# Performance work log

Measured on AMD Instinct MI355X. Metric: run time of the kernel, lower is better.

## Reference

```python
import jax, jax.numpy as jnp
import numpy as np

ENC_DIM = 128
DEC_DIM = 128
NUM_HEADS = 4
HEAD_DIM = DEC_DIM // NUM_HEADS


def _layernorm(x, g, b, eps=1e-5):
    mu = jnp.mean(x, axis=-1, keepdims=True)
    var = jnp.mean((x - mu) ** 2, axis=-1, keepdims=True)
    return (x - mu) * jax.lax.rsqrt(var + eps) * g + b


def setup_inputs() -> dict:
    key = jax.random.key(0)
    ks = jax.random.split(key, 12)
    B, H, W, D = 2, 16, 16, 16
    s = 0.02
    return {
        "encoder_feat": jax.random.normal(ks[0], (B, ENC_DIM, H, W, D), jnp.float32),
        "decoder_feat": jax.random.normal(ks[1], (B, DEC_DIM, H, W, D), jnp.float32),
        # torch Linear weights stored as [out, in]
        "Wq": jax.random.normal(ks[2], (DEC_DIM, DEC_DIM), jnp.float32) * s,
        "bq": jnp.zeros((DEC_DIM,), jnp.float32),
        "Wk": jax.random.normal(ks[3], (DEC_DIM, ENC_DIM), jnp.float32) * s,
        "bk": jnp.zeros((DEC_DIM,), jnp.float32),
        "Wv": jax.random.normal(ks[4], (DEC_DIM, ENC_DIM), jnp.float32) * s,
        "bv": jnp.zeros((DEC_DIM,), jnp.float32),
        "Wo": jax.random.normal(ks[5], (DEC_DIM, DEC_DIM), jnp.float32) * s,
        "bo": jnp.zeros((DEC_DIM,), jnp.float32),
        "g_enc": jnp.ones((ENC_DIM,), jnp.float32),
        "b_enc": jnp.zeros((ENC_DIM,), jnp.float32),
        "g_dec": jnp.ones((DEC_DIM,), jnp.float32),
        "b_dec": jnp.zeros((DEC_DIM,), jnp.float32),
        "g_out": jnp.ones((DEC_DIM,), jnp.float32),
        "b_out": jnp.zeros((DEC_DIM,), jnp.float32),
        "W1": jax.random.normal(ks[6], (DEC_DIM * 4, DEC_DIM), jnp.float32) * s,
        "b1": jnp.zeros((DEC_DIM * 4,), jnp.float32),
        "W2": jax.random.normal(ks[7], (DEC_DIM, DEC_DIM * 4), jnp.float32) * s,
        "b2": jnp.zeros((DEC_DIM,), jnp.float32),
    }


def reference(encoder_feat, decoder_feat, Wq, bq, Wk, bk, Wv, bv, Wo, bo,
              g_enc, b_enc, g_dec, b_dec, g_out, b_out, W1, b1, W2, b2):
    B, C_dec, H, W_, D = decoder_feat.shape
    N = H * W_ * D
    scale = HEAD_DIM ** -0.5
    # [B, C, H, W, D] -> [B, N, C]
    enc_seq = encoder_feat.reshape(B, -1, N).transpose(0, 2, 1)
    dec_seq = decoder_feat.reshape(B, C_dec, N).transpose(0, 2, 1)
    enc_seq = _layernorm(enc_seq, g_enc, b_enc)
    dec_seq = _layernorm(dec_seq, g_dec, b_dec)
    # projections (torch Linear: x @ W.T + b), split heads -> [B, h, N, d]
    Q = (dec_seq @ Wq.T + bq).reshape(B, N, NUM_HEADS, HEAD_DIM).transpose(0, 2, 1, 3)
    K = (enc_seq @ Wk.T + bk).reshape(B, N, NUM_HEADS, HEAD_DIM).transpose(0, 2, 1, 3)
    V = (enc_seq @ Wv.T + bv).reshape(B, N, NUM_HEADS, HEAD_DIM).transpose(0, 2, 1, 3)
    attn = jnp.einsum('bhqd,bhkd->bhqk', Q, K) * scale  # [B, h, N, N]
    attn = jax.nn.softmax(attn, axis=-1)
    out = jnp.einsum('bhqk,bhkd->bhqd', attn, V)
    out = out.transpose(0, 2, 1, 3).reshape(B, N, C_dec)
    out = out @ Wo.T + bo
    out = dec_seq + out
    h = _layernorm(out, g_out, b_out)
    ffn = jax.nn.gelu(h @ W1.T + b1, approximate=False) @ W2.T + b2
    out = out + ffn
    return out.transpose(0, 2, 1).reshape(B, C_dec, H, W_, D)
```

## Files before the change

kernel.cpp:

```cpp
#include <hip/hip_runtime.h>
#include <hip/hip_bf16.h>
#include <math.h>

#define B_ 2
#define N_ 4096
#define BN_ 8192
#define NH_ 4
#define SPLIT_ 8

using bf16x8   = __attribute__((ext_vector_type(8))) __bf16;
using f32x4    = __attribute__((ext_vector_type(4))) float;
using ushortx8 = __attribute__((ext_vector_type(8))) unsigned short;

#if __has_builtin(__builtin_amdgcn_exp2f)
#define FAST_EXP2(x) __builtin_amdgcn_exp2f(x)
#else
#define FAST_EXP2(x) __expf((x) * 0.6931471805599453f)
#endif

static __device__ __forceinline__ unsigned short f2bf(float f) {
    union { __hip_bfloat16 h; unsigned short u; } c;
    c.h = __float2bfloat16(f);
    return c.u;
}
static __device__ __forceinline__ float bf2f(unsigned short u) {
    union { __hip_bfloat16 h; unsigned short u; } c;
    c.u = u;
    return __bfloat162float(c.h);
}
static __device__ __forceinline__ unsigned int pk2bf(float lo, float hi) {
    return __builtin_amdgcn_perm(__float_as_uint(hi) + 0x8000u,
                                 __float_as_uint(lo) + 0x8000u, 0x07060302u);
}

__global__ __launch_bounds__(256)
void qkv4_kernel(const float* __restrict__ enc, const float* __restrict__ dec,
                 const float* __restrict__ g_enc, const float* __restrict__ b_enc,
                 const float* __restrict__ g_dec, const float* __restrict__ b_dec,
                 const float* __restrict__ Wq, const float* __restrict__ Wk,
                 const float* __restrict__ Wv,
                 const float* __restrict__ bq, const float* __restrict__ bk,
                 const float* __restrict__ bv,
                 const float* __restrict__ Wo, const float* __restrict__ W1,
                 const float* __restrict__ W2,
                 unsigned short* __restrict__ wo, unsigned short* __restrict__ w1,
                 unsigned short* __restrict__ w2,
                 unsigned short* __restrict__ Qh, unsigned short* __restrict__ Kh,
                 unsigned short* __restrict__ Vt,
                 unsigned short* __restrict__ dec_lnb) {
    const int t = threadIdx.x;
    if (blockIdx.x >= 768) {
        const int e = ((int)blockIdx.x - 768) * 2048 + t * 8;
        const float* src; unsigned short* dst; int off;
        if (e < 16384)       { src = Wo; dst = wo; off = e; }
        else if (e < 81920)  { src = W1; dst = w1; off = e - 16384; }
        else                 { src = W2; dst = w2; off = e - 81920; }
        const float4 a = *(const float4*)(src + off);
        const float4 b = *(const float4*)(src + off + 4);
        uint4 p;
        p.x = pk2bf(a.x, a.y); p.y = pk2bf(a.z, a.w);
        p.z = pk2bf(b.x, b.y); p.w = pk2bf(b.z, b.w);
        *(uint4*)(dst + off) = p;
        return;
    }
    __shared__ float tile[128][33];
    __shared__ float mu_s[32], inv_s[32];
    __shared__ alignas(16) unsigned short Wlds[128][136];
    const int z  = blockIdx.x >> 8;
    const int m0 = (blockIdx.x & 255) * 32;
    const int b  = m0 >> 12, n0 = m0 & 4095;
    const float* inb   = ((z == 0) ? dec : enc) + (size_t)b * 128 * N_;
    const float* gamma = (z == 0) ? g_dec : g_enc;
    const float* beta  = (z == 0) ? b_dec : b_enc;
    const float* Wb    = (z == 0) ? Wq : ((z == 1) ? Wk : Wv);

    {
        const int col = t & 31;
        const int r0  = t >> 5;
        #pragma unroll
        for (int j = 0; j < 16; ++j) {
            const int r = r0 + 8 * j;
            tile[r][col] = inb[(size_t)r * N_ + n0 + col];
        }
    }
    {
        #pragma unroll
        for (int i = 0; i < 8; ++i) {
            const int e   = (i * 256 + t) * 8;
            const int col = e >> 7, k = e & 127;
            const float4 wa = *(const float4*)(Wb + e);
            const float4 wb = *(const float4*)(Wb + e + 4);
            uint4 p;
            p.x = pk2bf(wa.x, wa.y); p.y = pk2bf(wa.z, wa.w);
            p.z = pk2bf(wb.x, wb.y); p.w = pk2bf(wb.z, wb.w);
            *(uint4*)&Wlds[col][k] = p;
        }
    }
    __syncthreads();
    {
        const int tok = t >> 3;
        const int ln  = t & 7;
        float s = 0.f, ss = 0.f;
        for (int c = ln; c < 128; c += 8) {
            const float x = tile[c][tok];
            s += x; ss += x * x;
        }
        for (int m = 1; m < 8; m <<= 1) {
            s  += __shfl_xor(s, m);
            ss += __shfl_xor(ss, m);
        }
        if (ln == 0) {
            const float mu  = s * (1.f / 128.f);
            mu_s[tok]  = mu;
            inv_s[tok] = rsqrtf(ss * (1.f / 128.f) - mu * mu + 1e-5f);
        }
    }
    __syncthreads();

    const int wvx = t >> 6, lane = t & 63;
    const int l15 = lane & 15, quad = lane >> 4;
    const int tokgrp  = (wvx & 1) * 16;
    const int colbase = (wvx >> 1) * 64;
    const bool wrLN   = (z == 0) && ((wvx >> 1) == 0);
    const int tok = tokgrp + l15;
    const float mu  = mu_s[tok];
    const float inv = inv_s[tok];

    bf16x8 af[4];
    #pragma unroll
    for (int kk = 0; kk < 4; ++kk) {
        float y[8];
        #pragma unroll
        for (int j = 0; j < 8; ++j) {
            const int c = kk * 32 + quad * 8 + j;
            y[j] = (tile[c][tok] - mu) * inv * gamma[c] + beta[c];
        }
        union { uint4 u; bf16x8 v8; ushortx8 us; } cvt;
        cvt.u.x = pk2bf(y[0], y[1]); cvt.u.y = pk2bf(y[2], y[3]);
        cvt.u.z = pk2bf(y[4], y[5]); cvt.u.w = pk2bf(y[6], y[7]);
        af[kk] = cvt.v8;
        if (wrLN)
            *(ushortx8*)(dec_lnb + (size_t)(m0 + tok) * 128 + kk * 32 + quad * 8) = cvt.us;
    }

    const float* bias = (z == 0) ? bq : ((z == 1) ? bk : bv);
    const float sc = (z == 0) ? (0.17677669529663687f * 1.4426950408889634f) : 1.f;
    const int nbase = n0 + tokgrp + quad * 4;

    #pragma unroll
    for (int nb = 0; nb < 4; ++nb) {
        const int col = colbase + nb * 16 + l15;
        f32x4 a = {0.f, 0.f, 0.f, 0.f};
        #pragma unroll
        for (int kk = 0; kk < 4; ++kk) {
            const bf16x8 wf = *(const bf16x8*)&Wlds[col][kk * 32 + quad * 8];
            a = __builtin_amdgcn_mfma_f32_16x16x32_bf16(af[kk], wf, a, 0, 0, 0);
        }
        const int h = col >> 5, d = col & 31;
        const float bz = bias[col];
        if (z == 2) {
            ushort4 pk;
            pk.x = f2bf(a[0] + bz);
            pk.y = f2bf(a[1] + bz);
            pk.z = f2bf(a[2] + bz);
            pk.w = f2bf(a[3] + bz);
            *(ushort4*)(Vt + ((size_t)(b * NH_ + h) * 32 + d) * N_ + nbase) = pk;
        } else {
            unsigned short* dst = (z == 0) ? Qh : Kh;
            #pragma unroll
            for (int r = 0; r < 4; ++r)
                dst[((size_t)(b * NH_ + h) * N_ + nbase + r) * 32 + d] = f2bf((a[r] + bz) * sc);
        }
    }
}

__global__ __launch_bounds__(512)
void attn_kernel7(const unsigned short* __restrict__ Qh,
                  const unsigned short* __restrict__ Kh,
                  const unsigned short* __restrict__ Vt,
                  unsigned short* __restrict__ ctx) {
    __shared__ alignas(16) unsigned short sP[8][64][72];
    __shared__ float ldsL[8][64];

    const int gid  = blockIdx.x;
    const int bh   = gid & 7;
    const int qblk = gid >> 3;
    const int t  = threadIdx.x;
    const int wvx = t >> 6, lane = t & 63;
    const int l15 = lane & 15, quad = lane >> 4;
    const int s = wvx;
    const int qw = qblk * 64;
    const size_t hbse = (size_t)bh * N_ * 32;

    bf16x8 qf[4];
    #pragma unroll
    for (int f = 0; f < 4; ++f)
        qf[f] = *(const bf16x8*)(Qh + hbse + (size_t)(qw + f * 16 + l15) * 32 + quad * 8);

    const unsigned short* Kp = Kh + hbse;
    const unsigned short* Vp = Vt + (size_t)bh * 32 * N_;

    f32x4 o0[4], o1[4];
    float l[4];
    #pragma unroll
    for (int f = 0; f < 4; ++f) {
        o0[f] = f32x4{0.f, 0.f, 0.f, 0.f};
        o1[f] = f32x4{0.f, 0.f, 0.f, 0.f};
        l[f] = 0.f;
    }
    const f32x4 zero = {0.f, 0.f, 0.f, 0.f};

    const int kbeg = s * (N_ / SPLIT_);
    const int kend = kbeg + (N_ / SPLIT_);

    bf16x8 kf[4];
    #pragma unroll
    for (int c = 0; c < 4; ++c)
        kf[c] = *(const bf16x8*)(Kp + (size_t)(kbeg + c * 16 + l15) * 32 + quad * 8);

    for (int k0 = kbeg; k0 < kend; k0 += 64) {
        bf16x8 va[2], vb[2];
        #pragma unroll
        for (int s2 = 0; s2 < 2; ++s2) {
            va[s2] = *(const bf16x8*)(Vp + (size_t)l15 * N_        + k0 + s2 * 32 + quad * 8);
            vb[s2] = *(const bf16x8*)(Vp + (size_t)(16 + l15) * N_ + k0 + s2 * 32 + quad * 8);
        }
        const int kn = (k0 + 64 < kend) ? (k0 + 64) : kbeg;
        bf16x8 kfn[4];
        #pragma unroll
        for (int c = 0; c < 4; ++c)
            kfn[c] = *(const bf16x8*)(Kp + (size_t)(kn + c * 16 + l15) * 32 + quad * 8);

        __builtin_amdgcn_s_setprio(1);
        #pragma unroll
        for (int f = 0; f < 4; ++f) {
            #pragma unroll
            for (int c = 0; c < 4; ++c) {
                const f32x4 sv = __builtin_amdgcn_mfma_f32_16x16x32_bf16(kf[c], qf[f], zero, 0, 0, 0);
                const float p0 = FAST_EXP2(sv[0]);
                const float p1 = FAST_EXP2(sv[1]);
                const float p2 = FAST_EXP2(sv[2]);
                const float p3 = FAST_EXP2(sv[3]);
                l[f] += (p0 + p1) + (p2 + p3);
                uint2 pk;
                pk.x = pk2bf(p0, p1);
                pk.y = pk2bf(p2, p3);
                *(uint2*)&sP[wvx][f * 16 + l15][c * 16 + quad * 4] = pk;
            }
        }
        __builtin_amdgcn_s_setprio(0);
        __builtin_amdgcn_s_setprio(1);
        #pragma unroll
        for (int f = 0; f < 4; ++f) {
            #pragma unroll
            for (int s2 = 0; s2 < 2; ++s2) {
                const bf16x8 pf = *(const bf16x8*)&sP[wvx][f * 16 + l15][s2 * 32 + quad * 8];
                o0[f] = __builtin_amdgcn_mfma_f32_16x16x32_bf16(va[s2], pf, o0[f], 0, 0, 0);
                o1[f] = __builtin_amdgcn_mfma_f32_16x16x32_bf16(vb[s2], pf, o1[f], 0, 0, 0);
            }
        }
        __builtin_amdgcn_s_setprio(0);
        #pragma unroll
        for (int c = 0; c < 4; ++c) kf[c] = kfn[c];
    }

    float lf4[4];
    #pragma unroll
    for (int f = 0; f < 4; ++f) {
        float lf = l[f];
        lf += __shfl_xor(lf, 16);
        lf += __shfl_xor(lf, 32);
        lf4[f] = lf;
    }

    __syncthreads();
    float* ldsO = (float*)&sP[0][0][0];
    #pragma unroll
    for (int f = 0; f < 4; ++f) {
        const int q = f * 16 + l15;
        float* row = ldsO + ((size_t)s * 64 + q) * 36;
        *(f32x4*)(row + quad * 4)      = o0[f];
        *(f32x4*)(row + 16 + quad * 4) = o1[f];
        if (quad == 0) ldsL[s][q] = lf4[f];
    }
    __syncthreads();

    const int tok = t >> 3;
    const int d0  = (t & 7) * 4;
    f32x4 sum = {0.f, 0.f, 0.f, 0.f};
    float lsum = 0.f;
    #pragma unroll
    for (int w = 0; w < 8; ++w) {
        sum  += *(const f32x4*)(ldsO + ((size_t)w * 64 + tok) * 36 + d0);
        lsum += ldsL[w][tok];
    }
    const float inv = 1.f / lsum;
    uint2 pk;
    pk.x = pk2bf(sum[0] * inv, sum[1] * inv);
    pk.y = pk2bf(sum[2] * inv, sum[3] * inv);
    const int b = bh >> 2, h = bh & 3;
    *(uint2*)(ctx + ((size_t)(b * N_ + qw + tok)) * 128 + h * 32 + d0) = pk;
}

__global__ __launch_bounds__(256)
void fused_tail4_kernel(const unsigned short* __restrict__ ctx,
                        const unsigned short* __restrict__ wo,
                        const float* __restrict__ bo,
                        const unsigned short* __restrict__ decb,
                        const float* __restrict__ g, const float* __restrict__ be,
                        const unsigned short* __restrict__ w1,
                        const float* __restrict__ b1,
                        const unsigned short* __restrict__ w2,
                        const float* __restrict__ b2,
                        float* __restrict__ out) {
    __shared__ alignas(16) unsigned short sredb[4][64][36];
    __shared__ float sln[4][2][16];
    __shared__ alignas(16) unsigned short hb_lds[16][136];
    __shared__ alignas(16) unsigned short smid[16][536];
    const int t = threadIdx.x;
    const int wv = t >> 6, lane = t & 63;
    const int l15 = lane & 15, quad = lane >> 4;
    const int m0 = blockIdx.x * 16;

    const int tokA = m0 + l15;
    const bf16x8 af = *(const bf16x8*)(ctx + (size_t)tokA * 128 + wv * 32 + quad * 8);

    #pragma unroll
    for (int nb = 0; nb < 8; ++nb) {
        const bf16x8 wf = *(const bf16x8*)(wo + (size_t)(nb * 16 + l15) * 128
                                           + wv * 32 + quad * 8);
        const f32x4 a = __builtin_amdgcn_mfma_f32_16x16x32_bf16(
            af, wf, f32x4{0.f, 0.f, 0.f, 0.f}, 0, 0, 0);
        uint2 p;
        p.x = pk2bf(a[0], a[1]);
        p.y = pk2bf(a[2], a[3]);
        *(uint2*)&sredb[wv][lane][nb * 4] = p;
    }
    __syncthreads();

    float v[2][4];
    #pragma unroll
    for (int lnb = 0; lnb < 2; ++lnb) {
        const int nbg = 2 * wv + lnb;
        f32x4 p = {0.f, 0.f, 0.f, 0.f};
        #pragma unroll
        for (int w = 0; w < 4; ++w) {
            const ushort4 u = *(const ushort4*)&sredb[w][lane][nbg * 4];
            p[0] += bf2f(u.x); p[1] += bf2f(u.y);
            p[2] += bf2f(u.z); p[3] += bf2f(u.w);
        }
        const int col = nbg * 16 + l15;
        const float bz = bo[col];
        #pragma unroll
        for (int r = 0; r < 4; ++r) {
            const int tok = m0 + quad * 4 + r;
            v[lnb][r] = p[r] + bz + bf2f(decb[(size_t)tok * 128 + col]);
        }
    }

    {
        float s[4], ss[4];
        #pragma unroll
        for (int r = 0; r < 4; ++r) {
            float a = v[0][r] + v[1][r];
            float b = v[0][r] * v[0][r] + v[1][r] * v[1][r];
            for (int m = 1; m < 16; m <<= 1) {
                a += __shfl_xor(a, m);
                b += __shfl_xor(b, m);
            }
            s[r] = a; ss[r] = b;
        }
        if (l15 == 0) {
            #pragma unroll
            for (int r = 0; r < 4; ++r) {
                sln[wv][0][quad * 4 + r] = s[r];
                sln[wv][1][quad * 4 + r] = ss[r];
            }
        }
    }
    __syncthreads();

    {
        #pragma unroll
        for (int r = 0; r < 4; ++r) {
            const int tk = quad * 4 + r;
            const float stot  = sln[0][0][tk] + sln[1][0][tk] + sln[2][0][tk] + sln[3][0][tk];
            const float sstot = sln[0][1][tk] + sln[1][1][tk] + sln[2][1][tk] + sln[3][1][tk];
            const float mu  = stot * (1.f / 128.f);
            const float inv = rsqrtf(sstot * (1.f / 128.f) - mu * mu + 1e-5f);
            #pragma unroll
            for (int lnb = 0; lnb < 2; ++lnb) {
                const int col = (2 * wv + lnb) * 16 + l15;
                hb_lds[tk][col] = f2bf((v[lnb][r] - mu) * inv * g[col] + be[col]);
            }
        }
    }
    __syncthreads();

    bf16x8 hf[4];
    #pragma unroll
    for (int kk = 0; kk < 4; ++kk)
        hf[kk] = *(const bf16x8*)&hb_lds[l15][kk * 32 + quad * 8];
    #pragma unroll
    for (int nb = 0; nb < 8; ++nb) {
        const int col = wv * 128 + nb * 16 + l15;
        f32x4 a = {0.f, 0.f, 0.f, 0.f};
        #pragma unroll
        for (int kk = 0; kk < 4; ++kk) {
            const bf16x8 wf = *(const bf16x8*)(w1 + (size_t)col * 128 + kk * 32 + quad * 8);
            a = __builtin_amdgcn_mfma_f32_16x16x32_bf16(hf[kk], wf, a, 0, 0, 0);
        }
        const float bz = b1[col];
        #pragma unroll
        for (int r = 0; r < 4; ++r) {
            float x = a[r] + bz;
            x = 0.5f * x * (1.f + erff(x * 0.70710678118f));
            smid[quad * 4 + r][col] = f2bf(x);
        }
    }
    __syncthreads();

    f32x4 acc[8];
    #pragma unroll
    for (int nb = 0; nb < 8; ++nb) acc[nb] = f32x4{0.f, 0.f, 0.f, 0.f};
    #pragma unroll
    for (int kk = 0; kk < 4; ++kk) {
        const bf16x8 af2 = *(const bf16x8*)&smid[l15][wv * 128 + kk * 32 + quad * 8];
        #pragma unroll
        for (int nb = 0; nb < 8; ++nb) {
            const bf16x8 wf = *(const bf16x8*)(w2 + (size_t)(nb * 16 + l15) * 512
                                               + wv * 128 + kk * 32 + quad * 8);
            acc[nb] = __builtin_amdgcn_mfma_f32_16x16x32_bf16(af2, wf, acc[nb], 0, 0, 0);
        }
    }
    __syncthreads();
    #pragma unroll
    for (int nb = 0; nb < 8; ++nb) {
        uint2 p;
        p.x = pk2bf(acc[nb][0], acc[nb][1]);
        p.y = pk2bf(acc[nb][2], acc[nb][3]);
        *(uint2*)&sredb[wv][lane][nb * 4] = p;
    }
    __syncthreads();

    {
        const int b = m0 >> 12;
        const int nb0 = (m0 & 4095) + quad * 4;
        #pragma unroll
        for (int lnb = 0; lnb < 2; ++lnb) {
            const int nbg = 2 * wv + lnb;
            f32x4 p = {0.f, 0.f, 0.f, 0.f};
            #pragma unroll
            for (int w = 0; w < 4; ++w) {
                const ushort4 u = *(const ushort4*)&sredb[w][lane][nbg * 4];
                p[0] += bf2f(u.x); p[1] += bf2f(u.y);
                p[2] += bf2f(u.z); p[3] += bf2f(u.w);
            }
            const int col = nbg * 16 + l15;
            const float bz = b2[col];
            f32x4 res;
            #pragma unroll
            for (int r = 0; r < 4; ++r)
                res[r] = p[r] + bz + v[lnb][r];
            *(f32x4*)&out[((size_t)(b * 128 + col)) * N_ + nb0] = res;
        }
    }
}

extern "C" void kernel_launch(void* const* d_in, const int* in_sizes, int n_in,
                              void* d_out, int out_size, void* d_ws, size_t ws_size,
                              hipStream_t stream) {
    const float* enc   = (const float*)d_in[0];
    const float* dec   = (const float*)d_in[1];
    const float* Wq    = (const float*)d_in[2];
    const float* bq    = (const float*)d_in[3];
    const float* Wk    = (const float*)d_in[4];
    const float* bk    = (const float*)d_in[5];
    const float* Wv    = (const float*)d_in[6];
    const float* bv    = (const float*)d_in[7];
    const float* Wo    = (const float*)d_in[8];
    const float* bo    = (const float*)d_in[9];
    const float* g_enc = (const float*)d_in[10];
    const float* b_enc = (const float*)d_in[11];
    const float* g_dec = (const float*)d_in[12];
    const float* b_dec = (const float*)d_in[13];
    const float* g_out = (const float*)d_in[14];
    const float* b_out = (const float*)d_in[15];
    const float* W1    = (const float*)d_in[16];
    const float* b1    = (const float*)d_in[17];
    const float* W2    = (const float*)d_in[18];
    const float* b2    = (const float*)d_in[19];
    float* out = (float*)d_out;
    char*  W   = (char*)d_ws;

    unsigned short* wob = (unsigned short*)(W);
    unsigned short* w1b = wob + 16384;
    unsigned short* w2b = w1b + 65536;
    unsigned short* dec_lnb = (unsigned short*)(W + (2560ull << 10));
    unsigned short* Qh      = (unsigned short*)(W + (4608ull << 10));
    unsigned short* Kh      = (unsigned short*)(W + (6656ull << 10));
    unsigned short* Vt      = (unsigned short*)(W + (8704ull << 10));
    unsigned short* ctx     = (unsigned short*)(W + (10752ull << 10));

    qkv4_kernel<<<768 + 72, 256, 0, stream>>>(
        enc, dec, g_enc, b_enc, g_dec, b_dec, Wq, Wk, Wv, bq, bk, bv,
        Wo, W1, W2, wob, w1b, w2b, Qh, Kh, Vt, dec_lnb);

    attn_kernel7<<<512, 512, 0, stream>>>(Qh, Kh, Vt, ctx);

    fused_tail4_kernel<<<512, 256, 0, stream>>>(ctx, wob, bo, dec_lnb,
                                                g_out, b_out, w1b, b1, w2b, b2, out);
}
```

Baseline: 157.1 us.

## Split tail GEMMs by output columns, fold weight conversion into QKV blocks

The tail kernel now has each wave own two output column blocks across the full K dimension for both the Wo and W2 GEMMs. This removes the split-K LDS reduction buffer, its bf16 round-trips and the extra barriers. The weight bf16 conversion is spread over the 768 QKV blocks, 24 threads each, instead of 72 extra blocks. The input tile load switches to float4 vector reads. In exchange, each wave now loads more weight data from global memory.

```diff
diff --git a/kernel.cpp b/kernel.cpp
--- a/kernel.cpp
+++ b/kernel.cpp
@@ -49,20 +49,6 @@
                  unsigned short* __restrict__ Vt,
                  unsigned short* __restrict__ dec_lnb) {
     const int t = threadIdx.x;
-    if (blockIdx.x >= 768) {
-        const int e = ((int)blockIdx.x - 768) * 2048 + t * 8;
-        const float* src; unsigned short* dst; int off;
-        if (e < 16384)       { src = Wo; dst = wo; off = e; }
-        else if (e < 81920)  { src = W1; dst = w1; off = e - 16384; }
-        else                 { src = W2; dst = w2; off = e - 81920; }
-        const float4 a = *(const float4*)(src + off);
-        const float4 b = *(const float4*)(src + off + 4);
-        uint4 p;
-        p.x = pk2bf(a.x, a.y); p.y = pk2bf(a.z, a.w);
-        p.z = pk2bf(b.x, b.y); p.w = pk2bf(b.z, b.w);
-        *(uint4*)(dst + off) = p;
-        return;
-    }
     __shared__ float tile[128][33];
     __shared__ float mu_s[32], inv_s[32];
     __shared__ alignas(16) unsigned short Wlds[128][136];
@@ -74,13 +60,29 @@
     const float* beta  = (z == 0) ? b_dec : b_enc;
     const float* Wb    = (z == 0) ? Wq : ((z == 1) ? Wk : Wv);
 
-    {
-        const int col = t & 31;
-        const int r0  = t >> 5;
-        #pragma unroll
-        for (int j = 0; j < 16; ++j) {
-            const int r = r0 + 8 * j;
-            tile[r][col] = inb[(size_t)r * N_ + n0 + col];
+    if (t < 24) {
+        const int e = (int)blockIdx.x * 192 + t * 8;
+        const float* src; unsigned short* dst; int off;
+        if (e < 16384)       { src = Wo; dst = wo; off = e; }
+        else if (e < 81920)  { src = W1; dst = w1; off = e - 16384; }
+        else                 { src = W2; dst = w2; off = e - 81920; }
+        const float4 a = *(const float4*)(src + off);
+        const float4 bq4 = *(const float4*)(src + off + 4);
+        uint4 p;
+        p.x = pk2bf(a.x, a.y); p.y = pk2bf(a.z, a.w);
+        p.z = pk2bf(bq4.x, bq4.y); p.w = pk2bf(bq4.z, bq4.w);
+        *(uint4*)(dst + off) = p;
+    }
+
+    {
+        const int r0 = t >> 3;
+        const int cf = (t & 7) * 4;
+        #pragma unroll
+        for (int j = 0; j < 4; ++j) {
+            const int r = r0 + 32 * j;
+            const float4 x = *(const float4*)(inb + (size_t)r * N_ + n0 + cf);
+            tile[r][cf]     = x.x; tile[r][cf + 1] = x.y;
+            tile[r][cf + 2] = x.z; tile[r][cf + 3] = x.w;
         }
     }
     {
@@ -303,7 +305,7 @@
 }
 
 __global__ __launch_bounds__(256)
-void fused_tail4_kernel(const unsigned short* __restrict__ ctx,
+void fused_tail5_kernel(const unsigned short* __restrict__ ctx,
                         const unsigned short* __restrict__ wo,
                         const float* __restrict__ bo,
                         const unsigned short* __restrict__ decb,
@@ -313,7 +315,6 @@
                         const unsigned short* __restrict__ w2,
                         const float* __restrict__ b2,
                         float* __restrict__ out) {
-    __shared__ alignas(16) unsigned short sredb[4][64][36];
     __shared__ float sln[4][2][16];
     __shared__ alignas(16) unsigned short hb_lds[16][136];
     __shared__ alignas(16) unsigned short smid[16][536];
@@ -322,39 +323,26 @@
     const int l15 = lane & 15, quad = lane >> 4;
     const int m0 = blockIdx.x * 16;
 
-    const int tokA = m0 + l15;
-    const bf16x8 af = *(const bf16x8*)(ctx + (size_t)tokA * 128 + wv * 32 + quad * 8);
-
-    #pragma unroll
-    for (int nb = 0; nb < 8; ++nb) {
-        const bf16x8 wf = *(const bf16x8*)(wo + (size_t)(nb * 16 + l15) * 128
-                                           + wv * 32 + quad * 8);
-        const f32x4 a = __builtin_amdgcn_mfma_f32_16x16x32_bf16(
-            af, wf, f32x4{0.f, 0.f, 0.f, 0.f}, 0, 0, 0);
-        uint2 p;
-        p.x = pk2bf(a[0], a[1]);
-        p.y = pk2bf(a[2], a[3]);
-        *(uint2*)&sredb[wv][lane][nb * 4] = p;
-    }
-    __syncthreads();
+    bf16x8 af[4];
+    #pragma unroll
+    for (int kk = 0; kk < 4; ++kk)
+        af[kk] = *(const bf16x8*)(ctx + (size_t)(m0 + l15) * 128 + kk * 32 + quad * 8);
 
     float v[2][4];
     #pragma unroll
     for (int lnb = 0; lnb < 2; ++lnb) {
-        const int nbg = 2 * wv + lnb;
-        f32x4 p = {0.f, 0.f, 0.f, 0.f};
-        #pragma unroll
-        for (int w = 0; w < 4; ++w) {
-            const ushort4 u = *(const ushort4*)&sredb[w][lane][nbg * 4];
-            p[0] += bf2f(u.x); p[1] += bf2f(u.y);
-            p[2] += bf2f(u.z); p[3] += bf2f(u.w);
-        }
-        const int col = nbg * 16 + l15;
+        const int col = (2 * wv + lnb) * 16 + l15;
+        f32x4 a = {0.f, 0.f, 0.f, 0.f};
+        #pragma unroll
+        for (int kk = 0; kk < 4; ++kk) {
+            const bf16x8 wf = *(const bf16x8*)(wo + (size_t)col * 128 + kk * 32 + quad * 8);
+            a = __builtin_amdgcn_mfma_f32_16x16x32_bf16(af[kk], wf, a, 0, 0, 0);
+        }
         const float bz = bo[col];
         #pragma unroll
         for (int r = 0; r < 4; ++r) {
             const int tok = m0 + quad * 4 + r;
-            v[lnb][r] = p[r] + bz + bf2f(decb[(size_t)tok * 128 + col]);
+            v[lnb][r] = a[r] + bz + bf2f(decb[(size_t)tok * 128 + col]);
         }
     }
 
@@ -420,48 +408,31 @@
     }
     __syncthreads();
 
-    f32x4 acc[8];
-    #pragma unroll
-    for (int nb = 0; nb < 8; ++nb) acc[nb] = f32x4{0.f, 0.f, 0.f, 0.f};
-    #pragma unroll
-    for (int kk = 0; kk < 4; ++kk) {
-        const bf16x8 af2 = *(const bf16x8*)&smid[l15][wv * 128 + kk * 32 + quad * 8];
-        #pragma unroll
-        for (int nb = 0; nb < 8; ++nb) {
-            const bf16x8 wf = *(const bf16x8*)(w2 + (size_t)(nb * 16 + l15) * 512
-                                               + wv * 128 + kk * 32 + quad * 8);
-            acc[nb] = __builtin_amdgcn_mfma_f32_16x16x32_bf16(af2, wf, acc[nb], 0, 0, 0);
-        }
-    }
-    __syncthreads();
-    #pragma unroll
-    for (int nb = 0; nb < 8; ++nb) {
-        uint2 p;
-        p.x = pk2bf(acc[nb][0], acc[nb][1]);
-        p.y = pk2bf(acc[nb][2], acc[nb][3]);
-        *(uint2*)&sredb[wv][lane][nb * 4] = p;
-    }
-    __syncthreads();
+    f32x4 acc[2];
+    acc[0] = f32x4{0.f, 0.f, 0.f, 0.f};
+    acc[1] = f32x4{0.f, 0.f, 0.f, 0.f};
+    #pragma unroll
+    for (int kk = 0; kk < 16; ++kk) {
+        const bf16x8 af2 = *(const bf16x8*)&smid[l15][kk * 32 + quad * 8];
+        #pragma unroll
+        for (int lnb = 0; lnb < 2; ++lnb) {
+            const int col = (2 * wv + lnb) * 16 + l15;
+            const bf16x8 wf = *(const bf16x8*)(w2 + (size_t)col * 512 + kk * 32 + quad * 8);
+            acc[lnb] = __builtin_amdgcn_mfma_f32_16x16x32_bf16(af2, wf, acc[lnb], 0, 0, 0);
+        }
+    }
 
     {
         const int b = m0 >> 12;
         const int nb0 = (m0 & 4095) + quad * 4;
         #pragma unroll
         for (int lnb = 0; lnb < 2; ++lnb) {
-            const int nbg = 2 * wv + lnb;
-            f32x4 p = {0.f, 0.f, 0.f, 0.f};
-            #pragma unroll
-            for (int w = 0; w < 4; ++w) {
-                const ushort4 u = *(const ushort4*)&sredb[w][lane][nbg * 4];
-                p[0] += bf2f(u.x); p[1] += bf2f(u.y);
-                p[2] += bf2f(u.z); p[3] += bf2f(u.w);
-            }
-            const int col = nbg * 16 + l15;
+            const int col = (2 * wv + lnb) * 16 + l15;
             const float bz = b2[col];
             f32x4 res;
             #pragma unroll
             for (int r = 0; r < 4; ++r)
-                res[r] = p[r] + bz + v[lnb][r];
+                res[r] = acc[lnb][r] + bz + v[lnb][r];
             *(f32x4*)&out[((size_t)(b * 128 + col)) * N_ + nb0] = res;
         }
     }
@@ -502,12 +473,12 @@
     unsigned short* Vt      = (unsigned short*)(W + (8704ull << 10));
     unsigned short* ctx     = (unsigned short*)(W + (10752ull << 10));
 
-    qkv4_kernel<<<768 + 72, 256, 0, stream>>>(
+    qkv4_kernel<<<768, 256, 0, stream>>>(
         enc, dec, g_enc, b_enc, g_dec, b_dec, Wq, Wk, Wv, bq, bk, bv,
         Wo, W1, W2, wob, w1b, w2b, Qh, Kh, Vt, dec_lnb);
 
     attn_kernel7<<<512, 512, 0, stream>>>(Qh, Kh, Vt, ctx);
 
-    fused_tail4_kernel<<<512, 256, 0, stream>>>(ctx, wob, bo, dec_lnb,
+    fused_tail5_kernel<<<512, 256, 0, stream>>>(ctx, wob, bo, dec_lnb,
                                                 g_out, b_out, w1b, b1, w2b, b2, out);
 }
```

After: 159.1 us. No clear change (+1.3%).
